# Kernel optimization log

Measured on AMD Instinct MI355X. Metric: run time of the kernel, lower is better.

Reference implementation:

```python
import jax, jax.numpy as jnp
import numpy as np

CONF_THRES = 0.596
IOU_THRES = 0.45
MAX_WH = 4096.0
K_CAND = 512      # NMS candidate cap (static)
MAX_DET = 300     # padded detections per image
IMG = 768.0       # hw = x[1].shape[-2:] * 8 -> 96*8


def _bilinear(feat, y, x):
    # feat: [C,H,W]; y,x: [R,S] sample coords. torchvision-style bilinear w/ border handling.
    C, H, W = feat.shape
    valid = (y > -1.0) & (y < H) & (x > -1.0) & (x < W)
    y = jnp.clip(y, 0.0)
    x = jnp.clip(x, 0.0)
    y0 = jnp.minimum(jnp.floor(y), H - 1).astype(jnp.int32)
    x0 = jnp.minimum(jnp.floor(x), W - 1).astype(jnp.int32)
    y1 = jnp.minimum(y0 + 1, H - 1)
    x1 = jnp.minimum(x0 + 1, W - 1)
    ly = y - y0
    lx = x - x0
    hy = 1.0 - ly
    hx = 1.0 - lx
    f00 = feat[:, y0, x0]
    f01 = feat[:, y0, x1]
    f10 = feat[:, y1, x0]
    f11 = feat[:, y1, x1]
    val = hy * hx * f00 + hy * lx * f01 + ly * hx * f10 + ly * lx * f11
    return val * valid  # [C,R,S]


def _roi_align_1x1(feat, boxes, scale):
    # RoIAlign(output_size=1, aligned=False); adaptive sampling_ratio replaced by fixed 2x2 grid.
    b = boxes * scale
    x1, y1, x2, y2 = b[:, 0], b[:, 1], b[:, 2], b[:, 3]
    rw = jnp.maximum(x2 - x1, 1.0)
    rh = jnp.maximum(y2 - y1, 1.0)
    offs = jnp.array([0.25, 0.75], dtype=boxes.dtype)  # (i+0.5)/2
    ys = y1[:, None] + rh[:, None] * offs  # [R,2]
    xs = x1[:, None] + rw[:, None] * offs
    R = ys.shape[0]
    yy = jnp.broadcast_to(ys[:, :, None], (R, 2, 2)).reshape(R, 4)
    xx = jnp.broadcast_to(xs[:, None, :], (R, 2, 2)).reshape(R, 4)
    v = _bilinear(feat, yy, xx)  # [C,R,4]
    return v.mean(-1).T  # [R,C]


def _iou_matrix(b):
    area = (b[:, 2] - b[:, 0]) * (b[:, 3] - b[:, 1])
    lt = jnp.maximum(b[:, None, :2], b[None, :, :2])
    rb = jnp.minimum(b[:, None, 2:], b[None, :, 2:])
    wh = jnp.clip(rb - lt, 0.0)
    inter = wh[..., 0] * wh[..., 1]
    return inter / (area[:, None] + area[None, :] - inter + 1e-7)


def _nms_image(pred):
    # pred: [N, 5+nc]. yolov5 non_max_suppression, static-shape version.
    obj = pred[:, 4]
    conf_all = pred[:, 5:] * obj[:, None]
    conf = conf_all.max(-1)
    cls = jnp.argmax(conf_all, -1)
    xy = pred[:, :2]
    wh = pred[:, 2:4]
    boxes = jnp.concatenate([xy - wh / 2, xy + wh / 2], -1)  # xywh2xyxy
    valid = (obj > CONF_THRES) & (conf > CONF_THRES)
    score = jnp.where(valid, conf, 0.0)
    sc, idx = jax.lax.top_k(score, K_CAND)
    b = boxes[idx]
    c = cls[idx].astype(boxes.dtype)
    iou = _iou_matrix(b + c[:, None] * MAX_WH)  # per-class offset NMS
    ar = jnp.arange(K_CAND)

    def body(i, keep):
        sup = keep[i] & (iou[i] > IOU_THRES) & (ar > i)
        return keep & (~sup)

    keep = jax.lax.fori_loop(0, K_CAND, body, sc > 0.0)
    sc2 = jnp.where(keep, sc, 0.0)
    sc3, idx2 = jax.lax.top_k(sc2, MAX_DET)
    return b[idx2], sc3 > 0.0  # [MAX_DET,4], [MAX_DET]


def _per_image(pred, g1, g2, g3, g4, W1, b1, W2, b2):
    bbox, mask = _nms_image(pred)
    f = jnp.concatenate([
        _roi_align_1x1(g1, bbox, 1.0 / 8),
        _roi_align_1x1(g2, bbox, 1.0 / 16),
        _roi_align_1x1(g3, bbox, 1.0 / 32),
        _roi_align_1x1(g4, bbox, 1.0 / 64),
    ], axis=1)  # [MAX_DET, 1920]
    h = jax.nn.leaky_relu(f @ W1 + b1)
    h = jax.nn.leaky_relu(h @ W2 + b2)
    out = jnp.concatenate([bbox / IMG, h], axis=-1)  # [MAX_DET, 4+64]
    return out * mask[:, None].astype(out.dtype)


def setup_inputs() -> dict:
    key = jax.random.key(0)
    ks = jax.random.split(key, 9)
    B, N, NC = 8, 36720, 80
    r = jax.random.uniform(ks[0], (B, N, 5 + NC), dtype=jnp.float32)
    xy = r[..., :2] * IMG
    wh = r[..., 2:4] * 112.0 + 8.0
    preds = jnp.concatenate([xy, wh, r[..., 4:]], axis=-1)
    f1 = jax.random.normal(ks[1], (B, 128, 96, 96), dtype=jnp.float32)
    f2 = jax.random.normal(ks[2], (B, 256, 48, 48), dtype=jnp.float32)
    f3 = jax.random.normal(ks[3], (B, 512, 24, 24), dtype=jnp.float32)
    f4 = jax.random.normal(ks[4], (B, 1024, 12, 12), dtype=jnp.float32)
    W1 = jax.random.normal(ks[5], (1920, 64), dtype=jnp.float32) / np.sqrt(1920.0)
    b1 = jnp.zeros((64,), jnp.float32)
    W2 = jax.random.normal(ks[6], (64, 64), dtype=jnp.float32) / 8.0
    b2 = jnp.zeros((64,), jnp.float32)
    return {"preds": preds, "f1": f1, "f2": f2, "f3": f3, "f4": f4,
            "W1": W1, "b1": b1, "W2": W2, "b2": b2}


def reference(preds, f1, f2, f3, f4, W1, b1, W2, b2):
    fn = lambda p, a, b_, c, d: _per_image(p, a, b_, c, d, W1, b1, W2, b2)
    return jax.vmap(fn)(preds, f1, f2, f3, f4)  # [B, MAX_DET, 68]
```

## Files before the change

### kernel.cpp

```cpp
#include <hip/hip_runtime.h>
#include <cstdint>

#define B_IMG   8
#define NCAND   36720
#define PD      85
#define NCLS    80
#define KC      512
#define MAXDET  300
#define NBUCK   2048
#define CANDCAP 1024

#define G2_OFF 4718592
#define G3_OFF 5898240
#define G4_OFF 6193152
#define G_TOT  6266880

#define P2_BASE 0
#define P2_SLAB 1179648
#define P3_BASE 2359296
#define P3_SLAB 294912
#define P4_BASE 3538944
#define P4_SLAB 73728

typedef unsigned int u32;
typedef unsigned long long u64;

__device__ __forceinline__ float leaky(float x){ return x >= 0.f ? x : 0.01f*x; }

__device__ __forceinline__ u64 shfl_u64(u64 v, int lane){
  int lo = __shfl((int)(u32)(v & 0xFFFFFFFFull), lane, 64);
  int hi = __shfl((int)(u32)(v >> 32), lane, 64);
  return ((u64)(u32)hi << 32) | (u64)(u32)lo;
}
__device__ __forceinline__ u64 shfl_xor_u64(u64 v, int mask){
  int lo = __shfl_xor((int)(u32)(v & 0xFFFFFFFFull), mask, 64);
  int hi = __shfl_xor((int)(u32)(v >> 32), mask, 64);
  return ((u64)(u32)hi << 32) | (u64)(u32)lo;
}

__device__ __forceinline__ void gld16(const void* g, void* l){
  __builtin_amdgcn_global_load_lds((const __attribute__((address_space(1))) void*)g,
                                   (__attribute__((address_space(3))) void*)l, 16, 0, 0);
}

__device__ __forceinline__ void stage8(const float4* __restrict__ feat4,
    const float4* __restrict__ W14, long fbase, int hw4, int px04, int Woff,
    int c0, int tid, float4* FsD, float4* WsD){
  const int wb = tid & ~63;
  #pragma unroll
  for (int k = 0; k < 2; k++){
    int s = tid + k*256; int c = s >> 6, q = s & 63;
    int pq = px04 + q; if (pq >= hw4) pq = hw4 - 1;
    gld16(feat4 + fbase + (long)(c0 + c)*hw4 + pq, FsD + k*256 + wb);
  }
  if (tid < 128){
    int c = tid >> 4, q = tid & 15;
    gld16(W14 + (long)(Woff + c0 + c)*16 + q, WsD + wb);
  }
}

#define FMA_Q(S, W, A) \
  A.x = fmaf(S, W.x, A.x); A.y = fmaf(S, W.y, A.y); \
  A.z = fmaf(S, W.z, A.z); A.w = fmaf(S, W.w, A.w);

__global__ __launch_bounds__(256) void k_front(const float* __restrict__ preds,
    u32* __restrict__ sbits, int* __restrict__ clsArr, u32* __restrict__ hist,
    const float* __restrict__ f1, const float* __restrict__ f2,
    const float* __restrict__ f3, const float* __restrict__ f4,
    const float* __restrict__ W1, float* __restrict__ G, float* __restrict__ P){
  __shared__ __align__(16) float smem[5120];
  const int img = blockIdx.y;
  const int u   = blockIdx.x;
  const int tid = threadIdx.x;

  if (u < 144){
    u32*   sl_lane = (u32*)smem;
    float* sl_obj  = smem + 256;
    u32*   sl_res  = (u32*)(smem + 512);
    u32*   sl_cls  = (u32*)(smem + 768);
    const int wv   = tid >> 6;
    const int lane = tid & 63;
    const int base = (u*4 + wv)*64;
    const int ci   = base + lane;
    const bool inb = ci < NCAND;
    float obj = 0.f;
    if (inb) obj = preds[((long)img*NCAND + ci)*PD + 4];
    const bool pass = obj > 0.596f;
    u64 mask = __ballot(pass);
    int cnt  = __popcll(mask);
    int rank = __popcll(mask & ((1ull << lane) - 1ull));
    if (pass){ sl_lane[wv*64 + rank] = (u32)lane; sl_obj[wv*64 + rank] = obj; }
    const int q = lane & 3;
    for (int r0 = 0; r0 < cnt; r0 += 16){
      int idx = r0 + (lane >> 2);
      if (idx < cnt){
        u32 sl = sl_lane[wv*64 + idx];
        float obj2 = sl_obj[wv*64 + idx];
        const float* p2 = preds + ((long)img*NCAND + base + (int)sl)*PD + 5 + q;
        u64 best = 0ull;
        #pragma unroll
        for (int k = 0; k < 20; k++){
          float v = p2[4*k] * obj2;
          u64 key = ((u64)__float_as_uint(v) << 32) | (u64)(~(u32)(q + 4*k));
          if (key > best) best = key;
        }
        u64 o1 = shfl_xor_u64(best, 1); if (o1 > best) best = o1;
        u64 o2 = shfl_xor_u64(best, 2); if (o2 > best) best = o2;
        if (q == 0){
          u32 bits = (u32)(best >> 32);
          sl_res[wv*64 + sl] = (__uint_as_float(bits) > 0.596f) ? bits : 0u;
          sl_cls[wv*64 + sl] = ~(u32)(best & 0xFFFFFFFFull);
        }
      }
    }
    if (inb){
      u32 out = pass ? sl_res[wv*64 + lane] : 0u;
      sbits[(long)img*NCAND + ci] = out;
      if (pass) clsArr[(long)img*NCAND + ci] = (int)sl_cls[wv*64 + lane];
      if (out) atomicAdd(&hist[img*NBUCK + ((out - 0x3F000000u) >> 12)], 1u);
    }
    return;
  }

  float4* Fs0 = (float4*)smem;
  float4* Fs1 = Fs0 + 512;
  float4* Ws0 = Fs0 + 1024;
  float4* Ws1 = Fs0 + 1152;
  const int v = u - 144;
  const float* feat; int C, HW, Woff, tile, split; long pbase; bool multi;
  if (v < 8)       { feat=f4; C=1024; HW=144;  Woff=896; tile=0;         split=v;
                     pbase=P4_BASE + (long)split*P4_SLAB; multi=true;  }
  else if (v < 20) { feat=f3; C=512;  HW=576;  Woff=384; tile=(v-8)>>2;  split=(v-8)&3;
                     pbase=P3_BASE + (long)split*P3_SLAB; multi=true;  }
  else if (v < 38) { feat=f2; C=256;  HW=2304; Woff=128; tile=(v-20)>>1; split=(v-20)&1;
                     pbase=P2_BASE + (long)split*P2_SLAB; multi=true;  }
  else             { feat=f1; C=128;  HW=9216; Woff=0;   tile=v-38;      split=0;
                     pbase=0; multi=false; }
  const int px0  = tile*256;
  const int hw4  = HW >> 2;
  const int px04 = px0 >> 2;
  const int jg   = tid & 7;
  const int pg   = tid >> 3;
  const int c0b  = split*128;
  const float4* feat4 = (const float4*)feat;
  const float4* W14   = (const float4*)W1;
  const long fbase = (long)img*C*hw4;
  float4 z = make_float4(0.f,0.f,0.f,0.f);
  float4 aA0=z,aA1=z,aA2=z,aA3=z,aA4=z,aA5=z,aA6=z,aA7=z;
  float4 aB0=z,aB1=z,aB2=z,aB3=z,aB4=z,aB5=z,aB6=z,aB7=z;

  stage8(feat4, W14, fbase, hw4, px04, Woff, c0b, tid, Fs0, Ws0);
  __syncthreads();
  for (int ch = 0; ch < 16; ch++){
    if (ch < 15)
      stage8(feat4, W14, fbase, hw4, px04, Woff, c0b + (ch+1)*8, tid,
             (ch & 1) ? Fs0 : Fs1, (ch & 1) ? Ws0 : Ws1);
    const float4* fsb = (ch & 1) ? Fs1 : Fs0;
    const float4* wsb = (ch & 1) ? Ws1 : Ws0;
    #pragma unroll
    for (int c = 0; c < 8; c++){
      float4 fa = fsb[c*64 + pg*2];
      float4 fb = fsb[c*64 + pg*2 + 1];
      float4 wa = wsb[c*16 + jg*2];
      float4 wc = wsb[c*16 + jg*2 + 1];
      FMA_Q(fa.x, wa, aA0) FMA_Q(fa.y, wa, aA1) FMA_Q(fa.z, wa, aA2) FMA_Q(fa.w, wa, aA3)
      FMA_Q(fb.x, wa, aA4) FMA_Q(fb.y, wa, aA5) FMA_Q(fb.z, wa, aA6) FMA_Q(fb.w, wa, aA7)
      FMA_Q(fa.x, wc, aB0) FMA_Q(fa.y, wc, aB1) FMA_Q(fa.z, wc, aB2) FMA_Q(fa.w, wc, aB3)
      FMA_Q(fb.x, wc, aB4) FMA_Q(fb.y, wc, aB5) FMA_Q(fb.z, wc, aB6) FMA_Q(fb.w, wc, aB7)
    }
    __syncthreads();
  }
  float* outb = multi ? (P + pbase + (long)img*HW*64)
                      : (G + (long)img*HW*64);
  const int pxa = px0 + pg*8;
#define STOREQ(A, B, PP) do { int gp = pxa + (PP); if (gp < HW){ \
    *(float4*)(outb + (long)gp*64 + jg*8) = A; \
    *(float4*)(outb + (long)gp*64 + jg*8 + 4) = B; } } while(0)
  STOREQ(aA0, aB0, 0); STOREQ(aA1, aB1, 1); STOREQ(aA2, aB2, 2); STOREQ(aA3, aB3, 3);
  STOREQ(aA4, aB4, 4); STOREQ(aA5, aB5, 5); STOREQ(aA6, aB6, 6); STOREQ(aA7, aB7, 7);
#undef STOREQ
}

__global__ __launch_bounds__(64) void k_thresh(const u32* __restrict__ hist,
                                               u32* __restrict__ thr){
  const int img = blockIdx.x;
  const int lane = threadIdx.x;
  const u32* h = hist + img*NBUCK;
  u32 acc = 0; u32 result = 0x3F000000u; bool found = false;
  for (int g = NBUCK/64 - 1; g >= 0 && !found; g--){
    u32 v = h[g*64 + lane];
    u32 s = v;
    #pragma unroll
    for (int off = 1; off < 64; off <<= 1){
      u32 t = __shfl_down(s, off, 64);
      s += (lane + off < 64) ? t : 0u;
    }
    u64 mask = __ballot(acc + s >= KC);
    if (mask){
      int hl = 63 - __clzll(mask);
      result = 0x3F000000u + ((u32)(g*64 + hl) << 12);
      found = true;
    }
    acc += __shfl(s, 0, 64);
  }
  if (lane == 0) thr[img] = result;
}

__global__ __launch_bounds__(256) void k_gather(const u32* __restrict__ sbits,
    const u32* __restrict__ thr, u32* __restrict__ cnt, u64* __restrict__ cand){
  int img = blockIdx.y;
  int n = blockIdx.x*256 + threadIdx.x;
  if (n >= NCAND) return;
  u32 bits = sbits[(long)img*NCAND + n];
  if (bits && bits >= thr[img]){
    u32 pos = atomicAdd(&cnt[img], 1u);
    if (pos < CANDCAP)
      cand[(long)img*CANDCAP + pos] = ((u64)bits << 32) | (u64)(0xFFFFFFFFu - (u32)n);
  }
}

__global__ __launch_bounds__(256) void k_mid(const float* __restrict__ preds,
    const int* __restrict__ clsArr, const u64* __restrict__ cand,
    const u32* __restrict__ cnt, float4* __restrict__ cbs_g,
    float4* __restrict__ obs_g, u64* __restrict__ kmask_g,
    const float4* __restrict__ P4f, float4* __restrict__ G4f){
#pragma clang fp contract(off)
  __shared__ __align__(16) u64 keys[CANDCAP];
  const int u   = blockIdx.x;
  const int tid = threadIdx.x;
  if (u < 32){
    const int img = u >> 2;
    const int sub = u & 3;
    const int M = min((int)cnt[img], CANDCAP);
    #pragma unroll
    for (int k = 0; k < 4; k++){
      int s = k*256 + tid;
      keys[s] = (s < M) ? cand[(long)img*CANDCAP + s] : 0ull;
    }
    __syncthreads();
    const int slot = sub*256 + tid;
    u64 k0 = keys[slot];
    int r0 = 0;
    const ulonglong2* kv = (const ulonglong2*)keys;
    for (int j = 0; j < CANDCAP/2; j++){
      ulonglong2 kk = kv[j];
      r0 += (kk.x > k0) + (kk.y > k0);
    }
    if ((k0 >> 32) != 0ull && r0 < KC){
      u32 idxn = 0xFFFFFFFFu - (u32)(k0 & 0xFFFFFFFFull);
      const float* p = preds + ((long)img*NCAND + idxn)*PD;
      float cx = p[0], cy = p[1], w = p[2], h = p[3];
      float hw = w*0.5f, hh = h*0.5f;
      float X1 = cx-hw, Y1 = cy-hh, X2 = cx+hw, Y2 = cy+hh;
      float off = (float)clsArr[(long)img*NCAND + idxn] * 4096.0f;
      obs_g[(long)img*KC + r0] = make_float4(X1, Y1, X2, Y2);
      cbs_g[(long)img*KC + r0] = make_float4(X1+off, Y1+off, X2+off, Y2+off);
      atomicOr(&kmask_g[img*8 + (r0 >> 6)], 1ull << (r0 & 63));
    }
    return;
  }
  const int N2 = P2_SLAB/4;
  const int N3 = P3_SLAB/4;
  const int N4 = P4_SLAB/4;
  int t = (u - 32)*256 + tid;
  if (t < N2){
    float4 a = P4f[t];
    float4 b = P4f[N2 + t];
    float4 r = make_float4(a.x+b.x, a.y+b.y, a.z+b.z, a.w+b.w);
    G4f[G2_OFF/4 + t] = r;
  } else if (t < N2 + N3){
    int w = t - N2;
    const float4* base = P4f + P3_BASE/4 + w;
    float4 r = base[0];
    #pragma unroll
    for (int s = 1; s < 4; s++){
      float4 b = base[(long)s*N3];
      r.x += b.x; r.y += b.y; r.z += b.z; r.w += b.w;
    }
    G4f[G3_OFF/4 + w] = r;
  } else if (t < N2 + N3 + N4){
    int w = t - N2 - N3;
    const float4* base = P4f + P4_BASE/4 + w;
    float4 r = base[0];
    #pragma unroll
    for (int s = 1; s < 8; s++){
      float4 b = base[(long)s*N4];
      r.x += b.x; r.y += b.y; r.z += b.z; r.w += b.w;
    }
    G4f[G4_OFF/4 + w] = r;
  }
}

__global__ __launch_bounds__(512) void k_iou(const float4* __restrict__ cbs_g,
    const u64* __restrict__ kmask_g, u64* __restrict__ lrows_g){
#pragma clang fp contract(off)
  __shared__ __align__(16) float4 cbsL[8*65];
  const int img = blockIdx.x >> 3;
  const int ch  = blockIdx.x & 7;
  const int tid = threadIdx.x;
  if (tid < KC){
    u64 km = kmask_g[img*8 + (tid >> 6)];
    bool f = (km >> (tid & 63)) & 1ull;
    float4 v = f ? cbs_g[(long)img*KC + tid]
                 : make_float4(-4e8f, -4e8f, -4e8f, -4e8f);
    cbsL[(tid >> 6)*65 + (tid & 63)] = v;
  }
  __syncthreads();
  const int row = ch*64 + (tid >> 3);
  const int w   = tid & 7;
  float4 bi = cbsL[(row >> 6)*65 + (row & 63)];
  float areai = (bi.z - bi.x)*(bi.w - bi.y);
  u64 bits = 0ull;
  const int jbase = w*64;
  for (int b = 0; b < 64; b++){
    int j = jbase + b;
    if (j > row){
      float4 bj = cbsL[w*65 + b];
      float areaj = (bj.z - bj.x)*(bj.w - bj.y);
      float ltx = fmaxf(bi.x, bj.x), lty = fmaxf(bi.y, bj.y);
      float rbx = fminf(bi.z, bj.z), rby = fminf(bi.w, bj.w);
      float ww = fmaxf(rbx - ltx, 0.f);
      float hh = fmaxf(rby - lty, 0.f);
      float inter = ww*hh;
      float iou = inter / (areai + areaj - inter + 1e-7f);
      if (iou > 0.45f) bits |= (1ull << b);
    }
  }
  lrows_g[((long)img*KC + row)*8 + w] = bits;
}

__global__ __launch_bounds__(512) void k_greedy(const u64* __restrict__ lrows_g,
    const u64* __restrict__ kmask_g, const float4* __restrict__ obs_g,
    float* __restrict__ selbox, u32* __restrict__ selcnt){
  __shared__ __align__(16) u64 lrows[KC*8];
  __shared__ u64 keepw[8];
  const int img = blockIdx.x;
  const int tid = threadIdx.x;
  const ulonglong2* src = (const ulonglong2*)(lrows_g + (long)img*KC*8);
  ulonglong2* dst = (ulonglong2*)lrows;
  #pragma unroll
  for (int k = 0; k < 4; k++) dst[k*512 + tid] = src[k*512 + tid];
  __syncthreads();
  if (tid < 64){
    const int lane = tid;
    const int w = lane & 7;
    u64 kw_own = kmask_g[img*8 + w];
    for (int b = 0; b < 8; b++){
      u64 kwb = shfl_u64(kw_own, b);
      for (int g = 0; g < 8; g++){
        u64 rdec[8], rown[8];
        #pragma unroll
        for (int k = 0; k < 8; k++){
          int i = b*64 + g*8 + k;
          rdec[k] = lrows[i*8 + b];
          rown[k] = lrows[i*8 + w];
        }
        #pragma unroll
        for (int k = 0; k < 8; k++){
          int il = g*8 + k;
          if ((kwb >> il) & 1ull){
            kwb    &= ~rdec[k];
            kw_own &= ~rown[k];
          }
        }
      }
    }
    if (lane < 8) keepw[lane] = kw_own;
  }
  __syncthreads();
  {
    u64 kk[8];
    #pragma unroll
    for (int w = 0; w < 8; w++) kk[w] = keepw[w];
    const int s = tid;
    const int wi = s >> 6, bi = s & 63;
    bool kept = (kk[wi] >> bi) & 1ull;
    if (kept){
      int rank = 0;
      for (int w = 0; w < wi; w++) rank += __popcll(kk[w]);
      rank += __popcll(bi ? (kk[wi] & ((1ull << bi) - 1ull)) : 0ull);
      if (rank < MAXDET){
        float4 ob = obs_g[(long)img*KC + s];
        float* sb = selbox + ((long)img*MAXDET + rank)*4;
        sb[0]=ob.x; sb[1]=ob.y; sb[2]=ob.z; sb[3]=ob.w;
      }
    }
    if (tid == 0){
      int tot = 0;
      #pragma unroll
      for (int w = 0; w < 8; w++) tot += __popcll(kk[w]);
      selcnt[img] = (u32)min(tot, MAXDET);
    }
  }
}

__device__ __forceinline__ void roi_level(const float* __restrict__ g,
    int Hl, int Wl, float scale, float x1, float y1, float x2, float y2,
    int lane, float& h){
  float bx1=x1*scale, by1=y1*scale, bx2=x2*scale, by2=y2*scale;
  float rw=fmaxf(bx2-bx1,1.f), rh=fmaxf(by2-by1,1.f);
  float ys[2]={by1+rh*0.25f, by1+rh*0.75f};
  float xs[2]={bx1+rw*0.25f, bx1+rw*0.75f};
  #pragma unroll
  for (int pt = 0; pt < 4; pt++){
    float y=ys[pt>>1], x=xs[pt&1];
    if ((y>-1.f)&&(y<(float)Hl)&&(x>-1.f)&&(x<(float)Wl)){
      float yc=fmaxf(y,0.f), xc=fmaxf(x,0.f);
      int y0=(int)fminf(floorf(yc),(float)(Hl-1));
      int x0=(int)fminf(floorf(xc),(float)(Wl-1));
      int y1i=min(y0+1,Hl-1), x1i=min(x0+1,Wl-1);
      float ly=yc-(float)y0, lx=xc-(float)x0;
      float hy=1.f-ly, hx=1.f-lx;
      h += (hy*hx*0.25f)*g[(long)(y0*Wl+x0)*64+lane];
      h += (hy*lx*0.25f)*g[(long)(y0*Wl+x1i)*64+lane];
      h += (ly*hx*0.25f)*g[(long)(y1i*Wl+x0)*64+lane];
      h += (ly*lx*0.25f)*g[(long)(y1i*Wl+x1i)*64+lane];
    }
  }
}

__global__ __launch_bounds__(256) void k_roi_mlp(const float* __restrict__ G,
    const float* __restrict__ selbox, const u32* __restrict__ selcnt,
    const float* __restrict__ b1, const float* __restrict__ W2,
    const float* __restrict__ b2, float* __restrict__ out){
  const int img  = blockIdx.y;
  const int wave = threadIdx.x >> 6;
  const int lane = threadIdx.x & 63;
  const int slot = blockIdx.x*4 + wave;
  if (slot >= MAXDET) return;
  float* o = out + ((long)img*MAXDET + slot)*68;
  if (slot >= (int)selcnt[img]){
    o[4+lane] = 0.f;
    if (lane < 4) o[lane] = 0.f;
    return;
  }
  const float* sb = selbox + ((long)img*MAXDET + slot)*4;
  float x1 = sb[0], y1 = sb[1], x2 = sb[2], y2 = sb[3];
  const float* Gi1 = G +          (long)img*9216*64;
  const float* Gi2 = G + G2_OFF + (long)img*2304*64;
  const float* Gi3 = G + G3_OFF + (long)img*576*64;
  const float* Gi4 = G + G4_OFF + (long)img*144*64;
  float h = 0.f;
  roi_level(Gi1, 96, 96, 0.125f,    x1,y1,x2,y2, lane, h);
  roi_level(Gi2, 48, 48, 0.0625f,   x1,y1,x2,y2, lane, h);
  roi_level(Gi3, 24, 24, 0.03125f,  x1,y1,x2,y2, lane, h);
  roi_level(Gi4, 12, 12, 0.015625f, x1,y1,x2,y2, lane, h);
  float h1 = leaky(h + b1[lane]);
  float c = 0.f;
  #pragma unroll 8
  for (int k = 0; k < 64; k++){
    float hk = __shfl(h1, k, 64);
    c += hk * W2[k*64 + lane];
  }
  o[4+lane] = leaky(c + b2[lane]);
  if (lane < 4) o[lane] = sb[lane] / 768.0f;
}

#define WS_G 2914048
#define WS_P 27981568

extern "C" void kernel_launch(void* const* d_in, const int* in_sizes, int n_in,
                              void* d_out, int out_size, void* d_ws, size_t ws_size,
                              hipStream_t stream){
  const float* preds = (const float*)d_in[0];
  const float* f1 = (const float*)d_in[1];
  const float* f2 = (const float*)d_in[2];
  const float* f3 = (const float*)d_in[3];
  const float* f4 = (const float*)d_in[4];
  const float* W1 = (const float*)d_in[5];
  const float* b1 = (const float*)d_in[6];
  const float* W2 = (const float*)d_in[7];
  const float* b2 = (const float*)d_in[8];
  float* out = (float*)d_out;
  char* ws = (char*)d_ws;
  u32* hist    = (u32*)(ws + 0);
  u32* cnt     = (u32*)(ws + 65536);
  u64* kmask_g = (u64*)(ws + 65792);
  u32* thr     = (u32*)(ws + 66304);
  float* selb  = (float*)(ws + 66560);
  u32* selc    = (u32*)(ws + 104960);
  u32* sbits   = (u32*)(ws + 105216);
  int* clsA    = (int*)(ws + 1280256);
  u64* cand    = (u64*)(ws + 2455296);
  float4* cbs_g = (float4*)(ws + 2520832);
  float4* obs_g = (float4*)(ws + 2586368);
  u64* lrows_g  = (u64*)(ws + 2651904);
  float* G     = (float*)(ws + WS_G);
  float* P     = (float*)(ws + WS_P);

  hipMemsetAsync(ws, 0, 66304, stream);

  k_front<<<dim3(218, B_IMG), 256, 0, stream>>>(preds, sbits, clsA, hist,
                                                f1, f2, f3, f4, W1, G, P);
  k_thresh<<<B_IMG, 64, 0, stream>>>(hist, thr);
  k_gather<<<dim3(144, B_IMG), 256, 0, stream>>>(sbits, thr, cnt, cand);
  k_mid<<<32 + 1512, 256, 0, stream>>>(preds, clsA, cand, cnt, cbs_g, obs_g,
                                       kmask_g, (const float4*)P, (float4*)G);
  k_iou<<<B_IMG*8, 512, 0, stream>>>(cbs_g, kmask_g, lrows_g);
  k_greedy<<<B_IMG, 512, 0, stream>>>(lrows_g, kmask_g, obs_g, selb, selc);
  k_roi_mlp<<<dim3(75, B_IMG), 256, 0, stream>>>(G, selb, selc, b1, W2, b2, out);
}
```

Measured before the change: 328.2 us.

## Split feature projection across two front kernels with smaller 128-thread blocks

Halves the projection tile to 128 pixels and 16-channel chunks, with 128-thread blocks. The projection work items are then interleaved between the scoring kernel and the gather kernel (even items in one, odd in the other), so the gather launch also carries compute and the load is spread across both kernels. The goal is better occupancy and balance across CUs. The cost is more blocks, more staging loads per FMA, and extra shared memory per block.

```diff
diff --git a/kernel.cpp b/kernel.cpp
--- a/kernel.cpp
+++ b/kernel.cpp
@@ -43,19 +43,20 @@
                                    (__attribute__((address_space(3))) void*)l, 16, 0, 0);
 }
 
-__device__ __forceinline__ void stage8(const float4* __restrict__ feat4,
+__device__ __forceinline__ void stage_chunk(const float4* __restrict__ feat4,
     const float4* __restrict__ W14, long fbase, int hw4, int px04, int Woff,
     int c0, int tid, float4* FsD, float4* WsD){
   const int wb = tid & ~63;
   #pragma unroll
+  for (int k = 0; k < 4; k++){
+    int s = tid + k*128; int c = s >> 5, q = s & 31;
+    int pq = px04 + q; if (pq >= hw4) pq = hw4 - 1;
+    gld16(feat4 + fbase + (long)(c0 + c)*hw4 + pq, FsD + k*128 + wb);
+  }
+  #pragma unroll
   for (int k = 0; k < 2; k++){
-    int s = tid + k*256; int c = s >> 6, q = s & 63;
-    int pq = px04 + q; if (pq >= hw4) pq = hw4 - 1;
-    gld16(feat4 + fbase + (long)(c0 + c)*hw4 + pq, FsD + k*256 + wb);
-  }
-  if (tid < 128){
-    int c = tid >> 4, q = tid & 15;
-    gld16(W14 + (long)(Woff + c0 + c)*16 + q, WsD + wb);
+    int s = tid + k*128; int c = s >> 4, q = s & 15;
+    gld16(W14 + (long)(Woff + c0 + c)*16 + q, WsD + k*128 + wb);
   }
 }
 
@@ -63,24 +64,87 @@
   A.x = fmaf(S, W.x, A.x); A.y = fmaf(S, W.y, A.y); \
   A.z = fmaf(S, W.z, A.z); A.w = fmaf(S, W.w, A.w);
 
-__global__ __launch_bounds__(256) void k_front(const float* __restrict__ preds,
+__device__ __forceinline__ void proj_work(int w, int img, int tid,
+    const float* __restrict__ f1, const float* __restrict__ f2,
+    const float* __restrict__ f3, const float* __restrict__ f4,
+    const float* __restrict__ W1, float* __restrict__ G, float* __restrict__ P,
+    float* smem){
+  float4* Fs0 = (float4*)smem;
+  float4* Fs1 = Fs0 + 512;
+  float4* Ws0 = Fs0 + 1024;
+  float4* Ws1 = Fs0 + 1280;
+  const float* feat; int C, HW, Woff, tile, split; long pbase; bool multi;
+  if (w < 16)      { feat=f4; C=1024; HW=144;  Woff=896; tile=w>>3;      split=w&7;
+                     pbase=P4_BASE + (long)split*P4_SLAB; multi=true;  }
+  else if (w < 36) { feat=f3; C=512;  HW=576;  Woff=384; tile=(w-16)>>2; split=(w-16)&3;
+                     pbase=P3_BASE + (long)split*P3_SLAB; multi=true;  }
+  else if (w < 72) { feat=f2; C=256;  HW=2304; Woff=128; tile=(w-36)>>1; split=(w-36)&1;
+                     pbase=P2_BASE + (long)split*P2_SLAB; multi=true;  }
+  else             { feat=f1; C=128;  HW=9216; Woff=0;   tile=w-72;      split=0;
+                     pbase=0; multi=false; }
+  const int px0  = tile*128;
+  const int hw4  = HW >> 2;
+  const int px04 = px0 >> 2;
+  const int jg   = tid & 7;
+  const int pg   = tid >> 3;
+  const int c0b  = split*128;
+  const float4* feat4 = (const float4*)feat;
+  const float4* W14   = (const float4*)W1;
+  const long fbase = (long)img*C*hw4;
+  float4 z = make_float4(0.f,0.f,0.f,0.f);
+  float4 aA0=z,aA1=z,aA2=z,aA3=z,aA4=z,aA5=z,aA6=z,aA7=z;
+  float4 aB0=z,aB1=z,aB2=z,aB3=z,aB4=z,aB5=z,aB6=z,aB7=z;
+
+  stage_chunk(feat4, W14, fbase, hw4, px04, Woff, c0b, tid, Fs0, Ws0);
+  __syncthreads();
+  for (int ch = 0; ch < 8; ch++){
+    if (ch < 7)
+      stage_chunk(feat4, W14, fbase, hw4, px04, Woff, c0b + (ch+1)*16, tid,
+                  (ch & 1) ? Fs0 : Fs1, (ch & 1) ? Ws0 : Ws1);
+    const float4* fsb = (ch & 1) ? Fs1 : Fs0;
+    const float4* wsb = (ch & 1) ? Ws1 : Ws0;
+    #pragma unroll 4
+    for (int c = 0; c < 16; c++){
+      float4 fa = fsb[c*32 + pg*2];
+      float4 fb = fsb[c*32 + pg*2 + 1];
+      float4 wa = wsb[c*16 + jg*2];
+      float4 wc = wsb[c*16 + jg*2 + 1];
+      FMA_Q(fa.x, wa, aA0) FMA_Q(fa.y, wa, aA1) FMA_Q(fa.z, wa, aA2) FMA_Q(fa.w, wa, aA3)
+      FMA_Q(fb.x, wa, aA4) FMA_Q(fb.y, wa, aA5) FMA_Q(fb.z, wa, aA6) FMA_Q(fb.w, wa, aA7)
+      FMA_Q(fa.x, wc, aB0) FMA_Q(fa.y, wc, aB1) FMA_Q(fa.z, wc, aB2) FMA_Q(fa.w, wc, aB3)
+      FMA_Q(fb.x, wc, aB4) FMA_Q(fb.y, wc, aB5) FMA_Q(fb.z, wc, aB6) FMA_Q(fb.w, wc, aB7)
+    }
+    __syncthreads();
+  }
+  float* outb = multi ? (P + pbase + (long)img*HW*64)
+                      : (G + (long)img*HW*64);
+  const int pxa = px0 + pg*8;
+#define STOREQ(A, B, PP) do { int gp = pxa + (PP); if (gp < HW){ \
+    *(float4*)(outb + (long)gp*64 + jg*8) = A; \
+    *(float4*)(outb + (long)gp*64 + jg*8 + 4) = B; } } while(0)
+  STOREQ(aA0, aB0, 0); STOREQ(aA1, aB1, 1); STOREQ(aA2, aB2, 2); STOREQ(aA3, aB3, 3);
+  STOREQ(aA4, aB4, 4); STOREQ(aA5, aB5, 5); STOREQ(aA6, aB6, 6); STOREQ(aA7, aB7, 7);
+#undef STOREQ
+}
+
+__global__ __launch_bounds__(128) void k_front_a(const float* __restrict__ preds,
     u32* __restrict__ sbits, int* __restrict__ clsArr, u32* __restrict__ hist,
     const float* __restrict__ f1, const float* __restrict__ f2,
     const float* __restrict__ f3, const float* __restrict__ f4,
     const float* __restrict__ W1, float* __restrict__ G, float* __restrict__ P){
-  __shared__ __align__(16) float smem[5120];
+  __shared__ __align__(16) float smem[6144];
   const int img = blockIdx.y;
   const int u   = blockIdx.x;
   const int tid = threadIdx.x;
 
-  if (u < 144){
+  if (u < 288){
     u32*   sl_lane = (u32*)smem;
-    float* sl_obj  = smem + 256;
-    u32*   sl_res  = (u32*)(smem + 512);
-    u32*   sl_cls  = (u32*)(smem + 768);
+    float* sl_obj  = smem + 128;
+    u32*   sl_res  = (u32*)(smem + 256);
+    u32*   sl_cls  = (u32*)(smem + 384);
     const int wv   = tid >> 6;
     const int lane = tid & 63;
-    const int base = (u*4 + wv)*64;
+    const int base = (u*2 + wv)*64;
     const int ci   = base + lane;
     const bool inb = ci < NCAND;
     float obj = 0.f;
@@ -121,64 +185,7 @@
     }
     return;
   }
-
-  float4* Fs0 = (float4*)smem;
-  float4* Fs1 = Fs0 + 512;
-  float4* Ws0 = Fs0 + 1024;
-  float4* Ws1 = Fs0 + 1152;
-  const int v = u - 144;
-  const float* feat; int C, HW, Woff, tile, split; long pbase; bool multi;
-  if (v < 8)       { feat=f4; C=1024; HW=144;  Woff=896; tile=0;         split=v;
-                     pbase=P4_BASE + (long)split*P4_SLAB; multi=true;  }
-  else if (v < 20) { feat=f3; C=512;  HW=576;  Woff=384; tile=(v-8)>>2;  split=(v-8)&3;
-                     pbase=P3_BASE + (long)split*P3_SLAB; multi=true;  }
-  else if (v < 38) { feat=f2; C=256;  HW=2304; Woff=128; tile=(v-20)>>1; split=(v-20)&1;
-                     pbase=P2_BASE + (long)split*P2_SLAB; multi=true;  }
-  else             { feat=f1; C=128;  HW=9216; Woff=0;   tile=v-38;      split=0;
-                     pbase=0; multi=false; }
-  const int px0  = tile*256;
-  const int hw4  = HW >> 2;
-  const int px04 = px0 >> 2;
-  const int jg   = tid & 7;
-  const int pg   = tid >> 3;
-  const int c0b  = split*128;
-  const float4* feat4 = (const float4*)feat;
-  const float4* W14   = (const float4*)W1;
-  const long fbase = (long)img*C*hw4;
-  float4 z = make_float4(0.f,0.f,0.f,0.f);
-  float4 aA0=z,aA1=z,aA2=z,aA3=z,aA4=z,aA5=z,aA6=z,aA7=z;
-  float4 aB0=z,aB1=z,aB2=z,aB3=z,aB4=z,aB5=z,aB6=z,aB7=z;
-
-  stage8(feat4, W14, fbase, hw4, px04, Woff, c0b, tid, Fs0, Ws0);
-  __syncthreads();
-  for (int ch = 0; ch < 16; ch++){
-    if (ch < 15)
-      stage8(feat4, W14, fbase, hw4, px04, Woff, c0b + (ch+1)*8, tid,
-             (ch & 1) ? Fs0 : Fs1, (ch & 1) ? Ws0 : Ws1);
-    const float4* fsb = (ch & 1) ? Fs1 : Fs0;
-    const float4* wsb = (ch & 1) ? Ws1 : Ws0;
-    #pragma unroll
-    for (int c = 0; c < 8; c++){
-      float4 fa = fsb[c*64 + pg*2];
-      float4 fb = fsb[c*64 + pg*2 + 1];
-      float4 wa = wsb[c*16 + jg*2];
-      float4 wc = wsb[c*16 + jg*2 + 1];
-      FMA_Q(fa.x, wa, aA0) FMA_Q(fa.y, wa, aA1) FMA_Q(fa.z, wa, aA2) FMA_Q(fa.w, wa, aA3)
-      FMA_Q(fb.x, wa, aA4) FMA_Q(fb.y, wa, aA5) FMA_Q(fb.z, wa, aA6) FMA_Q(fb.w, wa, aA7)
-      FMA_Q(fa.x, wc, aB0) FMA_Q(fa.y, wc, aB1) FMA_Q(fa.z, wc, aB2) FMA_Q(fa.w, wc, aB3)
-      FMA_Q(fb.x, wc, aB4) FMA_Q(fb.y, wc, aB5) FMA_Q(fb.z, wc, aB6) FMA_Q(fb.w, wc, aB7)
-    }
-    __syncthreads();
-  }
-  float* outb = multi ? (P + pbase + (long)img*HW*64)
-                      : (G + (long)img*HW*64);
-  const int pxa = px0 + pg*8;
-#define STOREQ(A, B, PP) do { int gp = pxa + (PP); if (gp < HW){ \
-    *(float4*)(outb + (long)gp*64 + jg*8) = A; \
-    *(float4*)(outb + (long)gp*64 + jg*8 + 4) = B; } } while(0)
-  STOREQ(aA0, aB0, 0); STOREQ(aA1, aB1, 1); STOREQ(aA2, aB2, 2); STOREQ(aA3, aB3, 3);
-  STOREQ(aA4, aB4, 4); STOREQ(aA5, aB5, 5); STOREQ(aA6, aB6, 6); STOREQ(aA7, aB7, 7);
-#undef STOREQ
+  proj_work((u - 288)*2, img, tid, f1, f2, f3, f4, W1, G, P, smem);
 }
 
 __global__ __launch_bounds__(64) void k_thresh(const u32* __restrict__ hist,
@@ -206,17 +213,27 @@
   if (lane == 0) thr[img] = result;
 }
 
-__global__ __launch_bounds__(256) void k_gather(const u32* __restrict__ sbits,
-    const u32* __restrict__ thr, u32* __restrict__ cnt, u64* __restrict__ cand){
-  int img = blockIdx.y;
-  int n = blockIdx.x*256 + threadIdx.x;
-  if (n >= NCAND) return;
-  u32 bits = sbits[(long)img*NCAND + n];
-  if (bits && bits >= thr[img]){
-    u32 pos = atomicAdd(&cnt[img], 1u);
-    if (pos < CANDCAP)
-      cand[(long)img*CANDCAP + pos] = ((u64)bits << 32) | (u64)(0xFFFFFFFFu - (u32)n);
-  }
+__global__ __launch_bounds__(128) void k_front_b(const u32* __restrict__ sbits,
+    const u32* __restrict__ thr, u32* __restrict__ cnt, u64* __restrict__ cand,
+    const float* __restrict__ f1, const float* __restrict__ f2,
+    const float* __restrict__ f3, const float* __restrict__ f4,
+    const float* __restrict__ W1, float* __restrict__ G, float* __restrict__ P){
+  __shared__ __align__(16) float smem[6144];
+  const int img = blockIdx.y;
+  const int u   = blockIdx.x;
+  const int tid = threadIdx.x;
+  if (u < 288){
+    int n = u*128 + tid;
+    if (n >= NCAND) return;
+    u32 bits = sbits[(long)img*NCAND + n];
+    if (bits && bits >= thr[img]){
+      u32 pos = atomicAdd(&cnt[img], 1u);
+      if (pos < CANDCAP)
+        cand[(long)img*CANDCAP + pos] = ((u64)bits << 32) | (u64)(0xFFFFFFFFu - (u32)n);
+    }
+    return;
+  }
+  proj_work((u - 288)*2 + 1, img, tid, f1, f2, f3, f4, W1, G, P, smem);
 }
 
 __global__ __launch_bounds__(256) void k_mid(const float* __restrict__ preds,
@@ -490,10 +507,11 @@
 
   hipMemsetAsync(ws, 0, 66304, stream);
 
-  k_front<<<dim3(218, B_IMG), 256, 0, stream>>>(preds, sbits, clsA, hist,
-                                                f1, f2, f3, f4, W1, G, P);
+  k_front_a<<<dim3(360, B_IMG), 128, 0, stream>>>(preds, sbits, clsA, hist,
+                                                  f1, f2, f3, f4, W1, G, P);
   k_thresh<<<B_IMG, 64, 0, stream>>>(hist, thr);
-  k_gather<<<dim3(144, B_IMG), 256, 0, stream>>>(sbits, thr, cnt, cand);
+  k_front_b<<<dim3(360, B_IMG), 128, 0, stream>>>(sbits, thr, cnt, cand,
+                                                  f1, f2, f3, f4, W1, G, P);
   k_mid<<<32 + 1512, 256, 0, stream>>>(preds, clsA, cand, cnt, cbs_g, obs_g,
                                        kmask_g, (const float4*)P, (float4*)G);
   k_iou<<<B_IMG*8, 512, 0, stream>>>(cbs_g, kmask_g, lrows_g);
```

Measured after the change: 335.4 us. +2.2%, slower.
